# Kernel optimization log

Measured on AMD Instinct MI355X. Metric: run time of the kernel, lower is better.

The kernel has to match this reference:

```python
import jax, jax.numpy as jnp
import numpy as np

EMBED_DIM = 512
NUM_HEADS = 8
HEAD_DIM = EMBED_DIM // NUM_HEADS  # 64


def setup_inputs() -> dict:
    key = jax.random.key(0)
    ks = jax.random.split(key, 11)
    B, S, E, dh = 4, 2048, EMBED_DIM, HEAD_DIM
    s_small = 1.0 / np.sqrt(dh)
    s_big = 1.0 / np.sqrt(E)
    return {
        "Q": jax.random.normal(ks[0], (B, S, E), jnp.float32),
        "K": jax.random.normal(ks[1], (B, S, E), jnp.float32),
        "V": jax.random.normal(ks[2], (B, S, E), jnp.float32),
        "Wq_w": jax.random.normal(ks[3], (dh, dh), jnp.float32) * s_small,
        "Wq_b": jnp.zeros((dh,), jnp.float32),
        "Wk_w": jax.random.normal(ks[4], (dh, dh), jnp.float32) * s_small,
        "Wk_b": jnp.zeros((dh,), jnp.float32),
        "Wv_w": jax.random.normal(ks[5], (dh, dh), jnp.float32) * s_small,
        "Wv_b": jnp.zeros((dh,), jnp.float32),
        "Wo_w": jax.random.normal(ks[6], (E, E), jnp.float32) * s_big,
        "Wo_b": jnp.zeros((E,), jnp.float32),
    }


def reference(Q, K, V, Wq_w, Wq_b, Wk_w, Wk_b, Wv_w, Wv_b, Wo_w, Wo_b):
    B, S, E = Q.shape
    H, dh = NUM_HEADS, HEAD_DIM
    # split heads: [B,S,E] -> [B,S,H,dh]; per-head shared linear (torch y = x @ W.T + b)
    q = jnp.einsum('bshd,od->bsho', Q.reshape(B, S, H, dh), Wq_w) + Wq_b
    k = jnp.einsum('bshd,od->bsho', K.reshape(B, S, H, dh), Wk_w) + Wk_b
    v = jnp.einsum('bshd,od->bsho', V.reshape(B, S, H, dh), Wv_w) + Wv_b
    # [B,H,S,dh]
    q = q.transpose(0, 2, 1, 3)
    k = k.transpose(0, 2, 1, 3)
    v = v.transpose(0, 2, 1, 3)
    scores = jnp.einsum('bhqd,bhkd->bhqk', q, k) / np.sqrt(dh)  # full N x N scores (faithful to naive impl)
    probs = jax.nn.softmax(scores, axis=-1)
    attn = jnp.einsum('bhqk,bhkd->bhqd', probs, v)
    # combine heads: [B,H,S,dh] -> [B,S,E]
    out = attn.transpose(0, 2, 1, 3).reshape(B, S, E)
    return out @ Wo_w.T + Wo_b
```

## Files before the change

### kernel.cpp

```cpp
#include <hip/hip_runtime.h>

typedef float  f32x4  __attribute__((ext_vector_type(4)));
typedef float  f32x16 __attribute__((ext_vector_type(16)));
typedef short  s16x8  __attribute__((ext_vector_type(8)));

constexpr int Bn = 4, Sn = 2048, En = 512, Hn = 8;
constexpr int BH = Bn * Hn;
constexpr int NT = Sn / 64;
constexpr float QSCL = 0.125f * 1.44269504088896f;

static __device__ __forceinline__ ushort f2bf(float f) {
  union { float f; uint u; } v; v.f = f;
  uint r = v.u + 0x7fffu + ((v.u >> 16) & 1u);
  return (ushort)(r >> 16);
}
static __device__ __forceinline__ uint2 pack4(float a, float b, float c, float d) {
  union { ushort us[4]; uint2 u; } pk;
  pk.us[0] = f2bf(a); pk.us[1] = f2bf(b); pk.us[2] = f2bf(c); pk.us[3] = f2bf(d);
  return pk.u;
}
static __device__ __forceinline__ float hexp2(float x) {
  float r; asm("v_exp_f32 %0, %1" : "=v"(r) : "v"(x)); return r;
}
static __device__ __forceinline__ uint pkbf(float lo, float hi2) {
  uint r; asm("v_cvt_pk_bf16_f32 %0, %1, %2" : "=v"(r) : "v"(lo), "v"(hi2)); return r;
}
#define SWAP32(a, b) asm("v_permlane32_swap_b32 %0, %1" : "+v"(a), "+v"(b))
static __device__ __forceinline__ s16x8 mk8(uint a, uint b, uint c, uint d) {
  union { uint u[4]; s16x8 v; } x; x.u[0] = a; x.u[1] = b; x.u[2] = c; x.u[3] = d; return x.v;
}
static __device__ __forceinline__ float vmax16(f32x16 v) {
  float a = fmaxf(fmaxf(v[0], v[1]), fmaxf(v[2], v[3]));
  float b = fmaxf(fmaxf(v[4], v[5]), fmaxf(v[6], v[7]));
  float c = fmaxf(fmaxf(v[8], v[9]), fmaxf(v[10], v[11]));
  float d = fmaxf(fmaxf(v[12], v[13]), fmaxf(v[14], v[15]));
  return fmaxf(fmaxf(a, b), fmaxf(c, d));
}
#define MFMA32(A, B, C) __builtin_amdgcn_mfma_f32_32x32x16_bf16((A), (B), (C), 0, 0, 0)
#define GLDS(SRC, DST) __builtin_amdgcn_global_load_lds( \
    (const __attribute__((address_space(1))) void*)(SRC), \
    (__attribute__((address_space(3))) void*)(DST), 16, 0, 0)

__global__ __launch_bounds__(256) void proj_kernel(
    const float* __restrict__ Qi, const float* __restrict__ Ki, const float* __restrict__ Vi,
    const float* __restrict__ Wq, const float* __restrict__ bq,
    const float* __restrict__ Wk, const float* __restrict__ bk,
    const float* __restrict__ Wv, const float* __restrict__ bv,
    ushort* __restrict__ qo, ushort* __restrict__ ko, ushort* __restrict__ vto)
{
  constexpr int LP = 72;
  __shared__ ushort Xl[64 * LP];
  __shared__ ushort Wl[64 * LP];
  const int role = blockIdx.z;
  const float* X    = role == 0 ? Qi : (role == 1 ? Ki : Vi);
  const float* W    = role == 0 ? Wq : (role == 1 ? Wk : Wv);
  const float* bias = role == 0 ? bq : (role == 1 ? bk : bv);
  const float oscl  = role == 0 ? QSCL : 1.0f;
  const int t = threadIdx.x, lane = t & 63, w = t >> 6;
  const int g = lane >> 4, ql = lane & 15;
  const int bh = blockIdx.y, b = bh >> 3, h = bh & 7;
  const int s0 = blockIdx.x * 64;

  {
    const int row = t >> 4, c = t & 15;
#pragma unroll
    for (int p = 0; p < 4; ++p) {
      const int rr = row + p * 16;
      const float4 wv = *(const float4*)(W + rr * 64 + c * 4);
      *(uint2*)&Wl[rr * LP + c * 4] = pack4(wv.x, wv.y, wv.z, wv.w);
      const float4 xv = *(const float4*)(X + ((size_t)b * Sn + s0 + rr) * En + h * 64 + c * 4);
      *(uint2*)&Xl[rr * LP + c * 4] = pack4(xv.x, xv.y, xv.z, xv.w);
    }
  }
  __syncthreads();

  f32x4 acc[4];
#pragma unroll
  for (int i = 0; i < 4; ++i) acc[i] = (f32x4){0.f, 0.f, 0.f, 0.f};
#pragma unroll
  for (int kc = 0; kc < 2; ++kc) {
    const s16x8 bfrag = *(const s16x8*)&Xl[(w * 16 + ql) * LP + kc * 32 + g * 8];
#pragma unroll
    for (int nt = 0; nt < 4; ++nt) {
      const s16x8 afrag = *(const s16x8*)&Wl[(nt * 16 + ql) * LP + kc * 32 + g * 8];
      acc[nt] = __builtin_amdgcn_mfma_f32_16x16x32_bf16(afrag, bfrag, acc[nt], 0, 0, 0);
    }
  }

  const int s = s0 + w * 16 + ql;
  if (role < 2) {
    ushort* dst = (role == 0 ? qo : ko) + ((size_t)bh * Sn + s) * 64;
#pragma unroll
    for (int nt = 0; nt < 4; ++nt) {
      const int ob = nt * 16 + g * 4;
      *(uint2*)&dst[ob] = pack4((acc[nt][0] + bias[ob]) * oscl, (acc[nt][1] + bias[ob + 1]) * oscl,
                                (acc[nt][2] + bias[ob + 2]) * oscl, (acc[nt][3] + bias[ob + 3]) * oscl);
    }
  } else {
#pragma unroll
    for (int nt = 0; nt < 4; ++nt) {
#pragma unroll
      for (int r = 0; r < 4; ++r) {
        const int o = nt * 16 + g * 4 + r;
        vto[((size_t)bh * 64 + o) * Sn + s] = f2bf(acc[nt][r] + bias[o]);
      }
    }
  }
}

__global__ __launch_bounds__(512, 4) void flash_kernel(
    const ushort* __restrict__ q, const ushort* __restrict__ k,
    const ushort* __restrict__ vt, ushort* __restrict__ attn)
{
  __shared__ __align__(16) char smem[36864];
  float* mrg = (float*)smem;
  const int tid = threadIdx.x, lane = tid & 63, w = tid >> 6;
  const int m = lane & 31, hi = lane >> 5;
  const int wl = w & 3, h2 = w >> 2;
  const int hx  = hi ^ (lane & 7);
  const int hxv = hx ^ (h2 << 2);

  int lid = blockIdx.x + (blockIdx.y << 4);
  lid = (lid & 7) * 64 + (lid >> 3);
  const int bq = lid & 15, bh = lid >> 4;
  const int qrow = bq * 128 + wl * 32 + m;
  const int b = bh >> 3, h = bh & 7;

  const ushort* qp = q + ((size_t)bh * Sn + qrow) * 64 + hi * 8;
  const s16x8 qf0 = *(const s16x8*)(qp + 0);
  const s16x8 qf1 = *(const s16x8*)(qp + 16);
  const s16x8 qf2 = *(const s16x8*)(qp + 32);
  const s16x8 qf3 = *(const s16x8*)(qp + 48);

  const int srow = tid >> 3, sc = tid & 7, scs = sc ^ (srow & 7);
  const ushort* kS = k  + (size_t)bh * Sn * 64 + (size_t)srow * 64 + scs * 8;
  const ushort* vS = vt + ((size_t)bh * 64 + srow) * Sn + scs * 8;
  const uint dO = (uint)(tid * 16);
  char* KB0 = smem;          char* KB1 = smem + 8192;
  char* VB0 = smem + 16384;  char* VB1 = smem + 24576;

  const f32x16 z16 = {};
  f32x16 acc0 = {}, acc1 = {};
  float mrun = -1e30f, lsum = 0.f;

  GLDS(kS, KB0 + dO); GLDS(vS, VB0 + dO);
  kS += 4096; vS += 64;

#define LDK(KB, S)     (*(const s16x8*)((KB)  + ((h2 * 32 + m) * 64 + (((2 * (S)) ^ hx ) << 3)) * 2))
#define LDV(VB, DT, S) (*(const s16x8*)((VB)  + (((DT) * 32 + m) * 64 + (((2 * (S)) ^ hxv) << 3)) * 2))

#define STEP(T, KB, VB, KBn, VBn) do {                                      \
    if ((T) < NT - 1) {                                                     \
      GLDS(kS, (KBn) + dO); GLDS(vS, (VBn) + dO);                           \
      kS += 4096; vS += 64;                                                 \
      asm volatile("s_waitcnt vmcnt(2)" ::: "memory");                      \
    } else {                                                                \
      asm volatile("s_waitcnt vmcnt(0)" ::: "memory");                      \
    }                                                                       \
    __builtin_amdgcn_s_barrier();                                           \
    __builtin_amdgcn_sched_barrier(0);                                      \
    f32x16 st;                                                              \
    __builtin_amdgcn_s_setprio(1);                                          \
    st = MFMA32(LDK(KB, 0), qf0, z16);                                      \
    st = MFMA32(LDK(KB, 1), qf1, st);                                       \
    st = MFMA32(LDK(KB, 2), qf2, st);                                       \
    st = MFMA32(LDK(KB, 3), qf3, st);                                       \
    __builtin_amdgcn_s_setprio(0);                                          \
    float tmax = vmax16(st);                                                \
    tmax = fmaxf(tmax, __shfl_xor(tmax, 32));                               \
    if (__any(tmax > mrun + 8.0f)) {                                        \
      const float mnew = fmaxf(mrun, tmax);                                 \
      const float rs = hexp2(mrun - mnew);                                  \
      mrun = mnew; lsum *= rs;                                              \
      _Pragma("unroll")                                                     \
      for (int i = 0; i < 16; ++i) { acc0[i] *= rs; acc1[i] *= rs; }        \
    }                                                                       \
    f32x16 p;                                                               \
    _Pragma("unroll")                                                       \
    for (int i = 0; i < 16; ++i) { p[i] = hexp2(st[i] - mrun); lsum += p[i]; } \
    uint uA, uB, uC, uD, uE, uF, uG, uH;                                    \
    uA = pkbf(p[0], p[1]);   uB = pkbf(p[4], p[5]);   SWAP32(uA, uB);       \
    uC = pkbf(p[2], p[3]);   uD = pkbf(p[6], p[7]);   SWAP32(uC, uD);       \
    uE = pkbf(p[8], p[9]);   uF = pkbf(p[12], p[13]); SWAP32(uE, uF);       \
    uG = pkbf(p[10], p[11]); uH = pkbf(p[14], p[15]); SWAP32(uG, uH);       \
    const s16x8 pb0 = mk8(uA, uC, uB, uD);                                  \
    const s16x8 pb1 = mk8(uE, uG, uF, uH);                                  \
    __builtin_amdgcn_s_setprio(1);                                          \
    acc0 = MFMA32(LDV(VB, 0, 0), pb0, acc0);                                \
    acc0 = MFMA32(LDV(VB, 0, 1), pb1, acc0);                                \
    acc1 = MFMA32(LDV(VB, 1, 0), pb0, acc1);                                \
    acc1 = MFMA32(LDV(VB, 1, 1), pb1, acc1);                                \
    __builtin_amdgcn_s_setprio(0);                                          \
    __builtin_amdgcn_s_barrier();                                           \
    __builtin_amdgcn_sched_barrier(0);                                      \
  } while (0)

  for (int T = 0; T < NT; T += 2) {
    STEP(T,     KB0, VB0, KB1, VB1);
    STEP(T + 1, KB1, VB1, KB0, VB0);
  }
#undef STEP
#undef LDK
#undef LDV

  const float lT = lsum + __shfl_xor(lsum, 32);
  float* mp = mrg + (size_t)(wl * 64 + lane) * 36;
  __syncthreads();
  if (h2) {
#pragma unroll
    for (int i = 0; i < 4; ++i) {
      f32x4 t0 = {acc0[4 * i], acc0[4 * i + 1], acc0[4 * i + 2], acc0[4 * i + 3]};
      f32x4 t1 = {acc1[4 * i], acc1[4 * i + 1], acc1[4 * i + 2], acc1[4 * i + 3]};
      *(f32x4*)(mp + 4 * i) = t0;
      *(f32x4*)(mp + 16 + 4 * i) = t1;
    }
    mp[32] = mrun; mp[33] = lT;
  }
  __syncthreads();
  if (!h2) {
    const float mU = mp[32], lU = mp[33];
    const float mM = fmaxf(mrun, mU);
    const float rL = hexp2(mrun - mM), rU = hexp2(mU - mM);
    const float inv = 1.0f / (lT * rL + lU * rU);
    const float sL = rL * inv, sU = rU * inv;
    ushort* ap = attn + ((size_t)(b * Sn + qrow)) * En + h * 64;
#pragma unroll
    for (int g2 = 0; g2 < 4; ++g2) {
      float a0 = acc0[g2 * 4 + 0] * sL + mp[g2 * 4 + 0] * sU;
      float a1 = acc0[g2 * 4 + 1] * sL + mp[g2 * 4 + 1] * sU;
      float a2 = acc0[g2 * 4 + 2] * sL + mp[g2 * 4 + 2] * sU;
      float a3 = acc0[g2 * 4 + 3] * sL + mp[g2 * 4 + 3] * sU;
      float c0 = acc1[g2 * 4 + 0] * sL + mp[16 + g2 * 4 + 0] * sU;
      float c1 = acc1[g2 * 4 + 1] * sL + mp[16 + g2 * 4 + 1] * sU;
      float c2 = acc1[g2 * 4 + 2] * sL + mp[16 + g2 * 4 + 2] * sU;
      float c3 = acc1[g2 * 4 + 3] * sL + mp[16 + g2 * 4 + 3] * sU;
      uint2 u0, u1;
      u0.x = pkbf(a0, a1); u0.y = pkbf(a2, a3);
      u1.x = pkbf(c0, c1); u1.y = pkbf(c2, c3);
      *(uint2*)&ap[g2 * 8 + hi * 4]      = u0;
      *(uint2*)&ap[32 + g2 * 8 + hi * 4] = u1;
    }
  }
}

__global__ __launch_bounds__(256) void outproj_kernel(
    const ushort* __restrict__ attn, const float* __restrict__ Wo,
    const float* __restrict__ bo, float* __restrict__ out)
{
  constexpr int LP = 72;
  __shared__ ushort Al[64 * LP];
  __shared__ ushort Wl[64 * LP];
  const int t = threadIdx.x, lane = t & 63, w = t >> 6;
  const int g = lane >> 4, ml = lane & 15;
  const int m0 = blockIdx.x * 64, n0 = blockIdx.y * 64;
  f32x4 acc[4];
#pragma unroll
  for (int i = 0; i < 4; ++i) acc[i] = (f32x4){0.f, 0.f, 0.f, 0.f};
  for (int e0 = 0; e0 < En; e0 += 64) {
    __syncthreads();
    {
      const int row = t >> 3, c = t & 7;
#pragma unroll
      for (int p = 0; p < 2; ++p) {
        const int rr = row + p * 32;
        const uint4 v = *(const uint4*)(attn + ((size_t)(m0 + rr)) * En + e0 + c * 8);
        *(uint4*)&Al[rr * LP + c * 8] = v;
      }
    }
    {
      const int row = t >> 4, c = t & 15;
#pragma unroll
      for (int p = 0; p < 4; ++p) {
        const int rr = row + p * 16;
        const float4 v = *(const float4*)(Wo + ((size_t)(n0 + rr)) * En + e0 + c * 4);
        *(uint2*)&Wl[rr * LP + c * 4] = pack4(v.x, v.y, v.z, v.w);
      }
    }
    __syncthreads();
#pragma unroll
    for (int kc = 0; kc < 2; ++kc) {
      const s16x8 bfrag = *(const s16x8*)&Al[(w * 16 + ml) * LP + kc * 32 + g * 8];
#pragma unroll
      for (int nt = 0; nt < 4; ++nt) {
        const s16x8 afrag = *(const s16x8*)&Wl[(nt * 16 + ml) * LP + kc * 32 + g * 8];
        acc[nt] = __builtin_amdgcn_mfma_f32_16x16x32_bf16(afrag, bfrag, acc[nt], 0, 0, 0);
      }
    }
  }
  const int mrow = m0 + w * 16 + ml;
#pragma unroll
  for (int nt = 0; nt < 4; ++nt) {
    const float4 bias = *(const float4*)(bo + n0 + nt * 16 + g * 4);
    float4 o;
    o.x = acc[nt][0] + bias.x;
    o.y = acc[nt][1] + bias.y;
    o.z = acc[nt][2] + bias.z;
    o.w = acc[nt][3] + bias.w;
    *(float4*)&out[(size_t)mrow * En + n0 + nt * 16 + g * 4] = o;
  }
}

extern "C" void kernel_launch(void* const* d_in, const int* in_sizes, int n_in,
                              void* d_out, int out_size, void* d_ws, size_t ws_size,
                              hipStream_t stream) {
  const float* Qi = (const float*)d_in[0];
  const float* Ki = (const float*)d_in[1];
  const float* Vi = (const float*)d_in[2];
  const float* Wq = (const float*)d_in[3];
  const float* bq = (const float*)d_in[4];
  const float* Wk = (const float*)d_in[5];
  const float* bk = (const float*)d_in[6];
  const float* Wv = (const float*)d_in[7];
  const float* bv = (const float*)d_in[8];
  const float* Wo = (const float*)d_in[9];
  const float* bo = (const float*)d_in[10];

  const size_t TEN = (size_t)BH * Sn * 64;
  ushort* qw  = (ushort*)d_ws;
  ushort* kw  = qw + TEN;
  ushort* vtw = kw + TEN;
  ushort* at  = vtw + TEN;

  proj_kernel<<<dim3(Sn / 64, BH, 3), 256, 0, stream>>>(
      Qi, Ki, Vi, Wq, bq, Wk, bk, Wv, bv, qw, kw, vtw);
  flash_kernel<<<dim3(16, 32), 512, 0, stream>>>(qw, kw, vtw, at);
  outproj_kernel<<<dim3(Bn * Sn / 64, En / 64), 256, 0, stream>>>(
      at, Wo, bo, (float*)d_out);
}
```

Before: 92.48 us.

## Halve flash block size, compute row sums via MFMA, restructure K/V prefetch sync

Flash attention blocks drop from 512 to 256 threads, each covering 64 query rows instead of 128, so twice as many blocks are launched with a remapped block-to-tile order. Each thread now issues two global-to-LDS loads per buffer, and the pipeline waits for all loads plus a barrier at the top of each step before prefetching the next tile, removing the trailing barrier. The softmax row sum is computed by an extra MFMA of the probabilities against a ones vector instead of scalar adds plus a lane shuffle. The max reduction tree is reshaped. Smaller blocks add more K/V reloads per head and a full vmcnt(0) wait each step, which may weaken load overlap.

```diff
diff --git a/kernel.cpp b/kernel.cpp
--- a/kernel.cpp
+++ b/kernel.cpp
@@ -30,11 +30,14 @@
   union { uint u[4]; s16x8 v; } x; x.u[0] = a; x.u[1] = b; x.u[2] = c; x.u[3] = d; return x.v;
 }
 static __device__ __forceinline__ float vmax16(f32x16 v) {
-  float a = fmaxf(fmaxf(v[0], v[1]), fmaxf(v[2], v[3]));
-  float b = fmaxf(fmaxf(v[4], v[5]), fmaxf(v[6], v[7]));
-  float c = fmaxf(fmaxf(v[8], v[9]), fmaxf(v[10], v[11]));
-  float d = fmaxf(fmaxf(v[12], v[13]), fmaxf(v[14], v[15]));
-  return fmaxf(fmaxf(a, b), fmaxf(c, d));
+  float a = fmaxf(fmaxf(v[0], v[1]), v[2]);
+  float b = fmaxf(fmaxf(v[3], v[4]), v[5]);
+  float c = fmaxf(fmaxf(v[6], v[7]), v[8]);
+  float d = fmaxf(fmaxf(v[9], v[10]), v[11]);
+  float e = fmaxf(fmaxf(v[12], v[13]), v[14]);
+  a = fmaxf(fmaxf(a, b), c);
+  d = fmaxf(fmaxf(d, e), v[15]);
+  return fmaxf(a, d);
 }
 #define MFMA32(A, B, C) __builtin_amdgcn_mfma_f32_32x32x16_bf16((A), (B), (C), 0, 0, 0)
 #define GLDS(SRC, DST) __builtin_amdgcn_global_load_lds( \
@@ -108,22 +111,22 @@
   }
 }
 
-__global__ __launch_bounds__(512, 4) void flash_kernel(
+__global__ __launch_bounds__(256, 4) void flash_kernel(
     const ushort* __restrict__ q, const ushort* __restrict__ k,
     const ushort* __restrict__ vt, ushort* __restrict__ attn)
 {
-  __shared__ __align__(16) char smem[36864];
+  __shared__ __align__(16) char smem[32768];
   float* mrg = (float*)smem;
   const int tid = threadIdx.x, lane = tid & 63, w = tid >> 6;
   const int m = lane & 31, hi = lane >> 5;
-  const int wl = w & 3, h2 = w >> 2;
-  const int hx  = hi ^ (lane & 7);
+  const int wl = w & 1, h2 = w >> 1;
+  const int hx  = hi ^ (m & 7);
   const int hxv = hx ^ (h2 << 2);
 
-  int lid = blockIdx.x + (blockIdx.y << 4);
-  lid = (lid & 7) * 64 + (lid >> 3);
-  const int bq = lid & 15, bh = lid >> 4;
-  const int qrow = bq * 128 + wl * 32 + m;
+  int lid = blockIdx.x + (blockIdx.y << 5);
+  lid = (lid & 7) * 128 + (lid >> 3);
+  const int bq = lid & 31, bh = lid >> 5;
+  const int qrow = bq * 64 + wl * 32 + m;
   const int b = bh >> 3, h = bh & 7;
 
   const ushort* qp = q + ((size_t)bh * Sn + qrow) * 64 + hi * 8;
@@ -132,32 +135,37 @@
   const s16x8 qf2 = *(const s16x8*)(qp + 32);
   const s16x8 qf3 = *(const s16x8*)(qp + 48);
 
-  const int srow = tid >> 3, sc = tid & 7, scs = sc ^ (srow & 7);
-  const ushort* kS = k  + (size_t)bh * Sn * 64 + (size_t)srow * 64 + scs * 8;
-  const ushort* vS = vt + ((size_t)bh * 64 + srow) * Sn + scs * 8;
-  const uint dO = (uint)(tid * 16);
+  const int scs = (lane & 7) ^ (lane >> 3);
+  const int r0 = w * 8 + (lane >> 3);
+  const ushort* kS = k  + (size_t)bh * Sn * 64 + (size_t)r0 * 64 + scs * 8;
+  const ushort* vS = vt + ((size_t)bh * 64 + r0) * Sn + scs * 8;
+  const uint dO = (uint)(w * 1024 + lane * 16);
   char* KB0 = smem;          char* KB1 = smem + 8192;
   char* VB0 = smem + 16384;  char* VB1 = smem + 24576;
 
   const f32x16 z16 = {};
-  f32x16 acc0 = {}, acc1 = {};
-  float mrun = -1e30f, lsum = 0.f;
-
-  GLDS(kS, KB0 + dO); GLDS(vS, VB0 + dO);
+  f32x16 acc0 = {}, acc1 = {}, asum = {};
+  float mrun = -1e30f;
+  union { ushort us[8]; s16x8 v; } onesU;
+#pragma unroll
+  for (int i = 0; i < 8; ++i) onesU.us[i] = 0x3F80;
+  const s16x8 ones = onesU.v;
+
+  GLDS(kS, KB0 + dO); GLDS(kS + 2048, KB0 + 4096 + dO);
+  GLDS(vS, VB0 + dO); GLDS(vS + (size_t)32 * Sn, VB0 + 4096 + dO);
   kS += 4096; vS += 64;
 
-#define LDK(KB, S)     (*(const s16x8*)((KB)  + ((h2 * 32 + m) * 64 + (((2 * (S)) ^ hx ) << 3)) * 2))
-#define LDV(VB, DT, S) (*(const s16x8*)((VB)  + (((DT) * 32 + m) * 64 + (((2 * (S)) ^ hxv) << 3)) * 2))
+#define LDK(KB, S)     (*(const s16x8*)((KB) + ((h2 * 32 + m) * 64 + (((2 * (S)) ^ hx ) << 3)) * 2))
+#define LDV(VB, DT, S) (*(const s16x8*)((VB) + (((DT) * 32 + m) * 64 + (((2 * (S)) ^ hxv) << 3)) * 2))
 
 #define STEP(T, KB, VB, KBn, VBn) do {                                      \
+    asm volatile("s_waitcnt vmcnt(0)" ::: "memory");                        \
+    __builtin_amdgcn_s_barrier();                                           \
     if ((T) < NT - 1) {                                                     \
-      GLDS(kS, (KBn) + dO); GLDS(vS, (VBn) + dO);                           \
+      GLDS(kS, (KBn) + dO); GLDS(kS + 2048, (KBn) + 4096 + dO);             \
+      GLDS(vS, (VBn) + dO); GLDS(vS + (size_t)32 * Sn, (VBn) + 4096 + dO);  \
       kS += 4096; vS += 64;                                                 \
-      asm volatile("s_waitcnt vmcnt(2)" ::: "memory");                      \
-    } else {                                                                \
-      asm volatile("s_waitcnt vmcnt(0)" ::: "memory");                      \
     }                                                                       \
-    __builtin_amdgcn_s_barrier();                                           \
     __builtin_amdgcn_sched_barrier(0);                                      \
     f32x16 st;                                                              \
     __builtin_amdgcn_s_setprio(1);                                          \
@@ -171,13 +179,13 @@
     if (__any(tmax > mrun + 8.0f)) {                                        \
       const float mnew = fmaxf(mrun, tmax);                                 \
       const float rs = hexp2(mrun - mnew);                                  \
-      mrun = mnew; lsum *= rs;                                              \
+      mrun = mnew; asum[0] *= rs;                                           \
       _Pragma("unroll")                                                     \
       for (int i = 0; i < 16; ++i) { acc0[i] *= rs; acc1[i] *= rs; }        \
     }                                                                       \
     f32x16 p;                                                               \
     _Pragma("unroll")                                                       \
-    for (int i = 0; i < 16; ++i) { p[i] = hexp2(st[i] - mrun); lsum += p[i]; } \
+    for (int i = 0; i < 16; ++i) p[i] = hexp2(st[i] - mrun);                \
     uint uA, uB, uC, uD, uE, uF, uG, uH;                                    \
     uA = pkbf(p[0], p[1]);   uB = pkbf(p[4], p[5]);   SWAP32(uA, uB);       \
     uC = pkbf(p[2], p[3]);   uD = pkbf(p[6], p[7]);   SWAP32(uC, uD);       \
@@ -190,9 +198,9 @@
     acc0 = MFMA32(LDV(VB, 0, 1), pb1, acc0);                                \
     acc1 = MFMA32(LDV(VB, 1, 0), pb0, acc1);                                \
     acc1 = MFMA32(LDV(VB, 1, 1), pb1, acc1);                                \
+    asum = MFMA32(ones, pb0, asum);                                         \
+    asum = MFMA32(ones, pb1, asum);                                         \
     __builtin_amdgcn_s_setprio(0);                                          \
-    __builtin_amdgcn_s_barrier();                                           \
-    __builtin_amdgcn_sched_barrier(0);                                      \
   } while (0)
 
   for (int T = 0; T < NT; T += 2) {
@@ -203,7 +211,7 @@
 #undef LDK
 #undef LDV
 
-  const float lT = lsum + __shfl_xor(lsum, 32);
+  const float lT = asum[0];
   float* mp = mrg + (size_t)(wl * 64 + lane) * 36;
   __syncthreads();
   if (h2) {
@@ -323,7 +331,7 @@
 
   proj_kernel<<<dim3(Sn / 64, BH, 3), 256, 0, stream>>>(
       Qi, Ki, Vi, Wq, bq, Wk, bk, Wv, bv, qw, kw, vtw);
-  flash_kernel<<<dim3(16, 32), 512, 0, stream>>>(qw, kw, vtw, at);
+  flash_kernel<<<dim3(32, 32), 256, 0, stream>>>(qw, kw, vtw, at);
   outproj_kernel<<<dim3(Bn * Sn / 64, En / 64), 256, 0, stream>>>(
       at, Wo, bo, (float*)d_out);
 }
```

Measured after the change: 97.01 us. 4.9% more time.
